# Kernel optimization log

Measured on AMD Instinct MI355X. Metric: run time of the kernel, lower is better.

The kernel has to match this reference:

```python
import jax, jax.numpy as jnp
import numpy as np

N_NODES = 50000
SCALE = 1.8  # fixed scale from the original module
EPS = 1e-12  # F.normalize eps


def setup_inputs() -> dict:
    key = jax.random.key(0)
    k1, k2, k3, k4 = jax.random.split(key, 4)
    in_ch, z_dim, E = 256, 64, 800000
    x = jax.random.normal(k1, (N_NODES, in_ch), dtype=jnp.float32)
    edge_index = jax.random.randint(k2, (2, E), 0, N_NODES, dtype=jnp.int64)
    # Linear params (PyTorch default init: U(-1/sqrt(fan_in), 1/sqrt(fan_in)))
    bound = 1.0 / np.sqrt(in_ch)
    W = jax.random.uniform(k3, (z_dim, in_ch), minval=-bound, maxval=bound, dtype=jnp.float32)
    b = jax.random.uniform(k4, (z_dim,), minval=-bound, maxval=bound, dtype=jnp.float32)
    return {"x": x, "W": W, "b": b, "edge_index": edge_index}


def reference(x, W, b, edge_index):
    N = x.shape[0]
    # linear + L2 normalize per node, scaled by 1.8
    h = x @ W.T + b  # [N, z]
    nrm = jnp.linalg.norm(h, axis=1, keepdims=True)
    h = h / jnp.maximum(nrm, EPS) * SCALE
    # APPNP K=1, alpha=0 with GCN normalization and added self-loops:
    # out = D^-1/2 (A + I) D^-1/2 h
    loop = jnp.arange(N, dtype=edge_index.dtype)
    src = jnp.concatenate([edge_index[0], loop])  # [E+N]
    dst = jnp.concatenate([edge_index[1], loop])
    ones = jnp.ones(src.shape[0], dtype=h.dtype)
    deg = jax.ops.segment_sum(ones, dst, num_segments=N)  # in-degree incl. self-loop
    dinv = jnp.where(deg > 0, deg ** -0.5, 0.0)
    coef = dinv[src] * dinv[dst]  # [E+N]
    msg = coef[:, None] * h[src]  # gather source features, weight per edge
    out = jax.ops.segment_sum(msg, dst, num_segments=N)  # scatter-sum to destinations
    return out
```

## Files before the change

kernel.cpp:

```cpp
#include <hip/hip_runtime.h>
#include <hip/hip_bf16.h>
#include <math.h>

#define ZD 64
#define IC 256
#define BSH 7
#define BCAP 2560
#define EPW 4096

using bf16x8 = __attribute__((ext_vector_type(8))) short;
using f32x4  = __attribute__((ext_vector_type(4))) float;

__device__ __forceinline__ short f2bf(float f) {
    __hip_bfloat16 h = __float2bfloat16(f);
    return *reinterpret_cast<short*>(&h);
}

__global__ __launch_bounds__(512) void k_init(unsigned* __restrict__ bcur, int NBK) {
    int t = threadIdx.x;
    if (t < NBK) bcur[t] = (unsigned)t * BCAP;
}

__global__ __launch_bounds__(256) void k_bin(const int* __restrict__ src,
                                             const int* __restrict__ dst, int E,
                                             unsigned* __restrict__ bcur,
                                             unsigned* __restrict__ binned, int NBK) {
    __shared__ unsigned hist[512], lbase[512], lcur[512];
    int t = threadIdx.x;
    for (int i = t; i < NBK; i += 256) { hist[i] = 0u; lcur[i] = 0u; }
    __syncthreads();
    int base = blockIdx.x * EPW;
#pragma unroll
    for (int i = 0; i < EPW / 256; ++i) {
        int e = base + i * 256 + t;
        if (e < E) atomicAdd(&hist[((unsigned)dst[e]) >> BSH], 1u);
    }
    __syncthreads();
    for (int i = t; i < NBK; i += 256) {
        unsigned c = hist[i];
        lbase[i] = c ? atomicAdd(&bcur[i], c) : 0u;
    }
    __syncthreads();
#pragma unroll
    for (int i = 0; i < EPW / 256; ++i) {
        int e = base + i * 256 + t;
        if (e < E) {
            unsigned d = (unsigned)dst[e];
            unsigned bk = d >> BSH;
            unsigned pos = lbase[bk] + atomicAdd(&lcur[bk], 1u);
            binned[pos] = (d << 16) | (unsigned)src[e];
        }
    }
}

__global__ __launch_bounds__(256) void k_deg2(const unsigned* __restrict__ bcur,
                                              const unsigned* __restrict__ binned,
                                              float* __restrict__ dinv, int N) {
    int b = blockIdx.x, t = threadIdx.x;
    __shared__ unsigned hist[128];
    if (t < 128) hist[t] = 0u;
    __syncthreads();
    unsigned cnt = bcur[b] - (unsigned)b * BCAP;
    const unsigned* recs = binned + (size_t)b * BCAP;
    for (unsigned i = t; i < cnt; i += 256)
        atomicAdd(&hist[(recs[i] >> 16) & 127u], 1u);
    __syncthreads();
    if (t < 128) {
        int node = b * 128 + t;
        if (node < N) dinv[node] = rsqrtf((float)hist[t] + 1.0f);
    }
}

__global__ __launch_bounds__(256) void k_packw(const float* __restrict__ W,
                                               unsigned short* __restrict__ Bpack) {
    int e = blockIdx.x * 256 + threadIdx.x;
    int j = e & 7;
    int lane = (e >> 3) & 63;
    int ct = (e >> 9) & 3;
    int s = e >> 11;
    int c = ct * 16 + (lane & 15);
    int k = s * 32 + (lane >> 4) * 8 + j;
    Bpack[e] = (unsigned short)f2bf(W[c * IC + k]);
}

__global__ __launch_bounds__(256) void k_linnorm_mfma(
    const float* __restrict__ x, const unsigned short* __restrict__ Bpack,
    const float* __restrict__ b, const float* __restrict__ dinv,
    float* __restrict__ g, int N) {
    __shared__ uint4 bp[2048];

    const uint4* bg = (const uint4*)Bpack;
#pragma unroll
    for (int i = 0; i < 8; ++i) bp[i * 256 + threadIdx.x] = bg[i * 256 + threadIdx.x];
    __syncthreads();

    int lane = threadIdx.x & 63;
    int w = threadIdx.x >> 6;
    int row0 = blockIdx.x * 64 + w * 16;
    if (row0 >= N) return;

    int r = lane & 15;
    int grp = lane >> 4;

    int rowA = row0 + r; if (rowA >= N) rowA = N - 1;
    const float* xr = x + (size_t)rowA * IC;

    f32x4 acc[4];
#pragma unroll
    for (int ct = 0; ct < 4; ++ct) {
        float bb = b[ct * 16 + r];
        acc[ct] = (f32x4){bb, bb, bb, bb};
    }

    const bf16x8* bpv = (const bf16x8*)bp;
#pragma unroll
    for (int s = 0; s < 8; ++s) {
        const float4* pa = (const float4*)(xr + s * 32 + grp * 8);
        float4 v0 = pa[0], v1 = pa[1];
        bf16x8 a;
        a[0] = f2bf(v0.x); a[1] = f2bf(v0.y); a[2] = f2bf(v0.z); a[3] = f2bf(v0.w);
        a[4] = f2bf(v1.x); a[5] = f2bf(v1.y); a[6] = f2bf(v1.z); a[7] = f2bf(v1.w);
#pragma unroll
        for (int ct = 0; ct < 4; ++ct) {
            bf16x8 bfr = bpv[(s * 4 + ct) * 64 + lane];
            acc[ct] = __builtin_amdgcn_mfma_f32_16x16x32_bf16(a, bfr, acc[ct], 0, 0, 0);
        }
    }

#pragma unroll
    for (int reg = 0; reg < 4; ++reg) {
        float ss = 0.f;
#pragma unroll
        for (int ct = 0; ct < 4; ++ct) ss += acc[ct][reg] * acc[ct][reg];
#pragma unroll
        for (int o = 1; o < 16; o <<= 1) ss += __shfl_xor(ss, o, 16);

        int rowg = row0 + grp * 4 + reg;
        int rc = rowg < N ? rowg : N - 1;
        float sc = 1.8f / fmaxf(sqrtf(ss), 1e-12f) * dinv[rc];
        if (rowg < N) {
            float* go = g + (size_t)rowg * ZD + r;
#pragma unroll
            for (int ct = 0; ct < 4; ++ct) go[ct * 16] = acc[ct][reg] * sc;
        }
    }
}

__global__ __launch_bounds__(256) void k_gather2(
    const unsigned* __restrict__ bcur, const unsigned* __restrict__ binned,
    const float* __restrict__ dinv, const float* __restrict__ g,
    float* __restrict__ out, int N) {
    int wg = blockIdx.x, b = wg >> 1, hf = wg & 1;
    __shared__ unsigned hist[64], rp[65], lcu[64];
    __shared__ unsigned short lcsr[2048];
    int t = threadIdx.x, lane = t & 63, w = t >> 6;
    if (t < 64) hist[t] = 0u;
    __syncthreads();

    unsigned cnt = bcur[b] - (unsigned)b * BCAP;
    const unsigned* recs = binned + (size_t)b * BCAP;

    for (unsigned i = t; i < cnt; i += 256) {
        unsigned dl = (recs[i] >> 16) & 127u;
        if ((int)(dl >> 6) == hf) atomicAdd(&hist[dl & 63u], 1u);
    }
    __syncthreads();
    if (w == 0) {
        unsigned v = hist[lane], incl = v;
#pragma unroll
        for (int d = 1; d < 64; d <<= 1) {
            unsigned u = __shfl_up(incl, d, 64);
            if (lane >= d) incl += u;
        }
        rp[lane + 1] = incl;
        if (lane == 0) rp[0] = 0u;
        lcu[lane] = incl - v;
    }
    __syncthreads();
    for (unsigned i = t; i < cnt; i += 256) {
        unsigned rec = recs[i];
        unsigned dl = (rec >> 16) & 127u;
        if ((int)(dl >> 6) == hf) {
            unsigned p = atomicAdd(&lcu[dl & 63u], 1u);
            lcsr[p] = (unsigned short)(rec & 0xFFFFu);
        }
    }
    __syncthreads();

    for (int q = 0; q < 16; ++q) {
        int nl = w * 16 + q;
        int node = b * 128 + hf * 64 + nl;
        if (node >= N) break;
        unsigned j = rp[nl], je = rp[nl + 1];
        float acc = g[(size_t)node * ZD + lane];
        for (; j + 8 <= je; j += 8) {
            unsigned short s0 = lcsr[j],     s1 = lcsr[j + 1];
            unsigned short s2 = lcsr[j + 2], s3 = lcsr[j + 3];
            unsigned short s4 = lcsr[j + 4], s5 = lcsr[j + 5];
            unsigned short s6 = lcsr[j + 6], s7 = lcsr[j + 7];
            float v0 = g[(size_t)s0 * ZD + lane], v1 = g[(size_t)s1 * ZD + lane];
            float v2 = g[(size_t)s2 * ZD + lane], v3 = g[(size_t)s3 * ZD + lane];
            float v4 = g[(size_t)s4 * ZD + lane], v5 = g[(size_t)s5 * ZD + lane];
            float v6 = g[(size_t)s6 * ZD + lane], v7 = g[(size_t)s7 * ZD + lane];
            acc += ((v0 + v1) + (v2 + v3)) + ((v4 + v5) + (v6 + v7));
        }
        for (; j < je; ++j) acc += g[(size_t)lcsr[j] * ZD + lane];
        out[(size_t)node * ZD + lane] = dinv[node] * acc;
    }
}

extern "C" void kernel_launch(void* const* d_in, const int* in_sizes, int n_in,
                              void* d_out, int out_size, void* d_ws, size_t ws_size,
                              hipStream_t stream) {
    const float* x = (const float*)d_in[0];
    const float* W = (const float*)d_in[1];
    const float* b = (const float*)d_in[2];
    const int* edge_index = (const int*)d_in[3];

    const int N = in_sizes[0] / IC;
    const int E = in_sizes[3] / 2;
    const int* src = edge_index;
    const int* dst = edge_index + E;
    float* out = (float*)d_out;

    const int NBK = (N + 127) >> BSH;

    char* p = (char*)d_ws;
    auto carve = [&](size_t bytes) {
        char* r = p;
        p += (bytes + 255) & ~(size_t)255;
        return r;
    };
    float*          g      = (float*)         carve((size_t)N * ZD * sizeof(float));
    float*          dinv   = (float*)         carve((size_t)N * sizeof(float));
    unsigned*       bcur   = (unsigned*)      carve(512 * sizeof(unsigned));
    unsigned short* Bpack  = (unsigned short*)carve(16384 * sizeof(unsigned short));
    unsigned*       binned = (unsigned*)      carve((size_t)NBK * BCAP * sizeof(unsigned));

    k_init<<<1, 512, 0, stream>>>(bcur, NBK);
    k_packw<<<64, 256, 0, stream>>>(W, Bpack);
    k_bin<<<(E + EPW - 1) / EPW, 256, 0, stream>>>(src, dst, E, bcur, binned, NBK);
    k_deg2<<<NBK, 256, 0, stream>>>(bcur, binned, dinv, N);
    k_linnorm_mfma<<<(N + 63) / 64, 256, 0, stream>>>(x, Bpack, b, dinv, g, N);
    k_gather2<<<2 * NBK, 256, 0, stream>>>(bcur, binned, dinv, g, out, N);
}
```

Baseline: 175.9 us.

## Store intermediate features in bf16, persist linear kernel grid, halve binning chunk

The normalized feature buffer g is now stored as bf16 instead of fp32, which halves the bytes moved by the random gather in the aggregation kernel. The linear+normalize kernel becomes a grid-stride loop over 260 blocks, so the 32 KB packed weight tile is loaded into LDS once per block rather than once per 64 rows. The edge binning chunk size is halved to launch more blocks. These are three separate ideas, and bf16 storage of g costs some accuracy in the summed outputs.

```diff
diff --git a/kernel.cpp b/kernel.cpp
--- a/kernel.cpp
+++ b/kernel.cpp
@@ -6,7 +6,7 @@
 #define IC 256
 #define BSH 7
 #define BCAP 2560
-#define EPW 4096
+#define EPW 2048
 
 using bf16x8 = __attribute__((ext_vector_type(8))) short;
 using f32x4  = __attribute__((ext_vector_type(4))) float;
@@ -14,6 +14,10 @@
 __device__ __forceinline__ short f2bf(float f) {
     __hip_bfloat16 h = __float2bfloat16(f);
     return *reinterpret_cast<short*>(&h);
+}
+__device__ __forceinline__ float bf2f(unsigned short u) {
+    unsigned v = ((unsigned)u) << 16;
+    return __builtin_bit_cast(float, v);
 }
 
 __global__ __launch_bounds__(512) void k_init(unsigned* __restrict__ bcur, int NBK) {
@@ -86,7 +90,7 @@
 __global__ __launch_bounds__(256) void k_linnorm_mfma(
     const float* __restrict__ x, const unsigned short* __restrict__ Bpack,
     const float* __restrict__ b, const float* __restrict__ dinv,
-    float* __restrict__ g, int N) {
+    unsigned short* __restrict__ g, int N) {
     __shared__ uint4 bp[2048];
 
     const uint4* bg = (const uint4*)Bpack;
@@ -96,59 +100,63 @@
 
     int lane = threadIdx.x & 63;
     int w = threadIdx.x >> 6;
-    int row0 = blockIdx.x * 64 + w * 16;
-    if (row0 >= N) return;
-
     int r = lane & 15;
     int grp = lane >> 4;
-
-    int rowA = row0 + r; if (rowA >= N) rowA = N - 1;
-    const float* xr = x + (size_t)rowA * IC;
-
-    f32x4 acc[4];
-#pragma unroll
-    for (int ct = 0; ct < 4; ++ct) {
-        float bb = b[ct * 16 + r];
-        acc[ct] = (f32x4){bb, bb, bb, bb};
-    }
-
     const bf16x8* bpv = (const bf16x8*)bp;
-#pragma unroll
-    for (int s = 0; s < 8; ++s) {
-        const float4* pa = (const float4*)(xr + s * 32 + grp * 8);
-        float4 v0 = pa[0], v1 = pa[1];
-        bf16x8 a;
-        a[0] = f2bf(v0.x); a[1] = f2bf(v0.y); a[2] = f2bf(v0.z); a[3] = f2bf(v0.w);
-        a[4] = f2bf(v1.x); a[5] = f2bf(v1.y); a[6] = f2bf(v1.z); a[7] = f2bf(v1.w);
+
+    int T = (N + 63) >> 6;
+    for (int tile = blockIdx.x; tile < T; tile += gridDim.x) {
+        int row0 = tile * 64 + w * 16;
+        if (row0 >= N) continue;
+
+        int rowA = row0 + r; if (rowA >= N) rowA = N - 1;
+        const float* xr = x + (size_t)rowA * IC;
+
+        f32x4 acc[4];
 #pragma unroll
         for (int ct = 0; ct < 4; ++ct) {
-            bf16x8 bfr = bpv[(s * 4 + ct) * 64 + lane];
-            acc[ct] = __builtin_amdgcn_mfma_f32_16x16x32_bf16(a, bfr, acc[ct], 0, 0, 0);
-        }
-    }
-
-#pragma unroll
-    for (int reg = 0; reg < 4; ++reg) {
-        float ss = 0.f;
-#pragma unroll
-        for (int ct = 0; ct < 4; ++ct) ss += acc[ct][reg] * acc[ct][reg];
-#pragma unroll
-        for (int o = 1; o < 16; o <<= 1) ss += __shfl_xor(ss, o, 16);
-
-        int rowg = row0 + grp * 4 + reg;
-        int rc = rowg < N ? rowg : N - 1;
-        float sc = 1.8f / fmaxf(sqrtf(ss), 1e-12f) * dinv[rc];
-        if (rowg < N) {
-            float* go = g + (size_t)rowg * ZD + r;
-#pragma unroll
-            for (int ct = 0; ct < 4; ++ct) go[ct * 16] = acc[ct][reg] * sc;
+            float bb = b[ct * 16 + r];
+            acc[ct] = (f32x4){bb, bb, bb, bb};
+        }
+
+#pragma unroll
+        for (int s = 0; s < 8; ++s) {
+            const float4* pa = (const float4*)(xr + s * 32 + grp * 8);
+            float4 v0 = pa[0], v1 = pa[1];
+            bf16x8 a;
+            a[0] = f2bf(v0.x); a[1] = f2bf(v0.y); a[2] = f2bf(v0.z); a[3] = f2bf(v0.w);
+            a[4] = f2bf(v1.x); a[5] = f2bf(v1.y); a[6] = f2bf(v1.z); a[7] = f2bf(v1.w);
+#pragma unroll
+            for (int ct = 0; ct < 4; ++ct) {
+                bf16x8 bfr = bpv[(s * 4 + ct) * 64 + lane];
+                acc[ct] = __builtin_amdgcn_mfma_f32_16x16x32_bf16(a, bfr, acc[ct], 0, 0, 0);
+            }
+        }
+
+#pragma unroll
+        for (int reg = 0; reg < 4; ++reg) {
+            float ss = 0.f;
+#pragma unroll
+            for (int ct = 0; ct < 4; ++ct) ss += acc[ct][reg] * acc[ct][reg];
+#pragma unroll
+            for (int o = 1; o < 16; o <<= 1) ss += __shfl_xor(ss, o, 16);
+
+            int rowg = row0 + grp * 4 + reg;
+            int rc = rowg < N ? rowg : N - 1;
+            float sc = 1.8f / fmaxf(sqrtf(ss), 1e-12f) * dinv[rc];
+            if (rowg < N) {
+                unsigned short* go = g + (size_t)rowg * ZD + r;
+#pragma unroll
+                for (int ct = 0; ct < 4; ++ct)
+                    go[ct * 16] = (unsigned short)f2bf(acc[ct][reg] * sc);
+            }
         }
     }
 }
 
 __global__ __launch_bounds__(256) void k_gather2(
     const unsigned* __restrict__ bcur, const unsigned* __restrict__ binned,
-    const float* __restrict__ dinv, const float* __restrict__ g,
+    const float* __restrict__ dinv, const unsigned short* __restrict__ g,
     float* __restrict__ out, int N) {
     int wg = blockIdx.x, b = wg >> 1, hf = wg & 1;
     __shared__ unsigned hist[64], rp[65], lcu[64];
@@ -192,19 +200,23 @@
         int node = b * 128 + hf * 64 + nl;
         if (node >= N) break;
         unsigned j = rp[nl], je = rp[nl + 1];
-        float acc = g[(size_t)node * ZD + lane];
+        float acc = bf2f(g[(size_t)node * ZD + lane]);
         for (; j + 8 <= je; j += 8) {
             unsigned short s0 = lcsr[j],     s1 = lcsr[j + 1];
             unsigned short s2 = lcsr[j + 2], s3 = lcsr[j + 3];
             unsigned short s4 = lcsr[j + 4], s5 = lcsr[j + 5];
             unsigned short s6 = lcsr[j + 6], s7 = lcsr[j + 7];
-            float v0 = g[(size_t)s0 * ZD + lane], v1 = g[(size_t)s1 * ZD + lane];
-            float v2 = g[(size_t)s2 * ZD + lane], v3 = g[(size_t)s3 * ZD + lane];
-            float v4 = g[(size_t)s4 * ZD + lane], v5 = g[(size_t)s5 * ZD + lane];
-            float v6 = g[(size_t)s6 * ZD + lane], v7 = g[(size_t)s7 * ZD + lane];
+            float v0 = bf2f(g[(size_t)s0 * ZD + lane]);
+            float v1 = bf2f(g[(size_t)s1 * ZD + lane]);
+            float v2 = bf2f(g[(size_t)s2 * ZD + lane]);
+            float v3 = bf2f(g[(size_t)s3 * ZD + lane]);
+            float v4 = bf2f(g[(size_t)s4 * ZD + lane]);
+            float v5 = bf2f(g[(size_t)s5 * ZD + lane]);
+            float v6 = bf2f(g[(size_t)s6 * ZD + lane]);
+            float v7 = bf2f(g[(size_t)s7 * ZD + lane]);
             acc += ((v0 + v1) + (v2 + v3)) + ((v4 + v5) + (v6 + v7));
         }
-        for (; j < je; ++j) acc += g[(size_t)lcsr[j] * ZD + lane];
+        for (; j < je; ++j) acc += bf2f(g[(size_t)lcsr[j] * ZD + lane]);
         out[(size_t)node * ZD + lane] = dinv[node] * acc;
     }
 }
@@ -231,7 +243,7 @@
         p += (bytes + 255) & ~(size_t)255;
         return r;
     };
-    float*          g      = (float*)         carve((size_t)N * ZD * sizeof(float));
+    unsigned short* g      = (unsigned short*)carve((size_t)N * ZD * sizeof(unsigned short));
     float*          dinv   = (float*)         carve((size_t)N * sizeof(float));
     unsigned*       bcur   = (unsigned*)      carve(512 * sizeof(unsigned));
     unsigned short* Bpack  = (unsigned short*)carve(16384 * sizeof(unsigned short));
@@ -241,6 +253,6 @@
     k_packw<<<64, 256, 0, stream>>>(W, Bpack);
     k_bin<<<(E + EPW - 1) / EPW, 256, 0, stream>>>(src, dst, E, bcur, binned, NBK);
     k_deg2<<<NBK, 256, 0, stream>>>(bcur, binned, dinv, N);
-    k_linnorm_mfma<<<(N + 63) / 64, 256, 0, stream>>>(x, Bpack, b, dinv, g, N);
+    k_linnorm_mfma<<<260, 256, 0, stream>>>(x, Bpack, b, dinv, g, N);
     k_gather2<<<2 * NBK, 256, 0, stream>>>(bcur, binned, dinv, g, out, N);
 }
```

Result: slower. 186.8 us (+6.2%).
